# Kernel tuning notes

Hardware: AMD Instinct MI355X
Metric: run time of the kernel (lower is better)

The kernel has to match this reference:

```python
import jax, jax.numpy as jnp
import numpy as np

NUM_HEADS = 20
MAX_SEQLEN = 1500  # max per-segment length (Whisper 30s -> 1500 frames); static for jit
NEG = -1e30


def setup_inputs() -> dict:
    key = jax.random.key(0)
    ks = jax.random.split(key, 6)
    B, S, D = 4, MAX_SEQLEN, 1280
    T = B * S
    hidden_states = jax.random.normal(ks[0], (T, D), dtype=jnp.float32)
    # packed varlen layout: 4 equal-length audio segments
    cu_seqlens = (jnp.arange(B + 1, dtype=jnp.int32) * S)
    w = 0.02
    Wq = jax.random.normal(ks[1], (D, D), dtype=jnp.float32) * w
    Wk = jax.random.normal(ks[2], (D, D), dtype=jnp.float32) * w
    Wv = jax.random.normal(ks[3], (D, D), dtype=jnp.float32) * w
    Wo = jax.random.normal(ks[4], (D, D), dtype=jnp.float32) * w
    bq = jnp.zeros((D,), jnp.float32)
    bv = jnp.zeros((D,), jnp.float32)
    bo = jnp.zeros((D,), jnp.float32)
    return {"hidden_states": hidden_states, "cu_seqlens": cu_seqlens,
            "Wq": Wq, "bq": bq, "Wk": Wk, "Wv": Wv, "bv": bv, "Wo": Wo, "bo": bo}


def _varlen_attention(hidden_states, cu_seqlens, Wq, bq, Wk, Wv, bv, Wo, bo):
    T, D = hidden_states.shape
    H = NUM_HEADS
    d = D // H
    scale = d ** -0.5
    S = MAX_SEQLEN
    B = cu_seqlens.shape[0] - 1

    # projections (torch nn.Linear convention: y = x @ W.T + b; k_proj has no bias)
    q = hidden_states @ Wq.T + bq   # [T, D]
    k = hidden_states @ Wk.T        # [T, D]
    v = hidden_states @ Wv.T + bv   # [T, D]

    lens = cu_seqlens[1:] - cu_seqlens[:-1]                 # [B]
    pos = jnp.arange(S, dtype=jnp.int32)                    # [S]
    valid = pos[None, :] < lens[:, None]                    # [B, S]
    idx = cu_seqlens[:-1, None] + pos[None, :]              # [B, S]
    idx_g = jnp.where(valid, idx, 0)

    # unpack to padded [B, S, H, d]
    qb = q[idx_g].reshape(B, S, H, d)
    kb = k[idx_g].reshape(B, S, H, d)
    vb = v[idx_g].reshape(B, S, H, d)

    scores = jnp.einsum('bqhd,bkhd->bhqk', qb, kb) * scale  # [B, H, S, S]
    scores = jnp.where(valid[:, None, None, :], scores, NEG)
    attn = jax.nn.softmax(scores, axis=-1)
    out = jnp.einsum('bhqk,bkhd->bqhd', attn, vb).reshape(B, S, D)

    # repack to [T, D]; invalid slots scatter out-of-bounds and are dropped
    idx_s = jnp.where(valid, idx, T).reshape(-1)
    packed = jnp.zeros((T, D), out.dtype).at[idx_s].set(out.reshape(-1, D), mode='drop')
    return packed @ Wo.T + bo


def reference(hidden_states, cu_seqlens, Wq, bq, Wk, Wv, bv, Wo, bo):
    return _varlen_attention(hidden_states, cu_seqlens, Wq, bq, Wk, Wv, bv, Wo, bo)
```

## Files before the change

### kernel.cpp

```cpp
#include <hip/hip_runtime.h>
#include <stdint.h>
#include <math.h>

#define DMODEL 1280
#define NHEAD  20
#define DHEAD  64
#define NSEG   4
#define MAXS   1500
#define SPAD   1536
#define TPAD   (NSEG*SPAD)
#define QT256  ((MAXS + 255) / 256)
#define BM 128
#define BN 128
#define BK 32
#define QSCALE 0.18033688011112042f
#define NEGV  -1e30f

typedef float  f32x4  __attribute__((ext_vector_type(4)));
typedef __bf16 bf16x8 __attribute__((ext_vector_type(8)));

#if __has_builtin(__builtin_amdgcn_exp2f)
#define EXP2F(x) __builtin_amdgcn_exp2f(x)
#else
#define EXP2F(x) exp2f(x)
#endif

__device__ __forceinline__ ushort f2bf(float f) {
  union { float f; uint32_t u; } a; a.f = f;
  uint32_t u = a.u;
  u += 0x7FFFu + ((u >> 16) & 1u);
  return (ushort)(u >> 16);
}

__device__ __forceinline__ uint32_t pk2(float a, float b) {
  union { float f; uint32_t u; } ua, ub; ua.f = a; ub.f = b;
  uint32_t x = ua.u + 0x8000u, y = ub.u + 0x8000u;
  return (x >> 16) | (y & 0xFFFF0000u);
}

__device__ __forceinline__ void async16(const void* g, void* lds) {
  __builtin_amdgcn_global_load_lds((const __attribute__((address_space(1))) void*)g,
                                   (__attribute__((address_space(3))) void*)lds,
                                   16, 0, 0);
}

__device__ __forceinline__ int perm32(int a) {
  return ((a >> 2) & 3) * 8 + ((a >> 4) & 1) * 4 + (a & 3);
}

__global__ void __launch_bounds__(256)
cvt_all(const float* __restrict__ hs, const float* __restrict__ Wq,
        const float* __restrict__ Wk, const float* __restrict__ Wv,
        const float* __restrict__ Wo, ushort* __restrict__ dst, int nX, int DD) {
  const int i = (blockIdx.x * 256 + threadIdx.x) * 4;
  const float* src;
  if (i < nX) {
    src = hs + i;
  } else {
    int j = i - nX;
    const int z = (j >= DD) + (j >= 2 * DD) + (j >= 3 * DD);
    const float* w = (z == 0) ? Wq : (z == 1) ? Wk : (z == 2) ? Wv : Wo;
    src = w + (j - z * DD);
  }
  float4 v = *(const float4*)src;
  ushort4 o;
  o.x = f2bf(v.x); o.y = f2bf(v.y); o.z = f2bf(v.z); o.w = f2bf(v.w);
  *(ushort4*)(dst + i) = o;
}

__device__ __forceinline__ void gemm_tile_mainloop(
    const ushort* __restrict__ A, const ushort* __restrict__ W,
    int M, int m0, int n0, ushort* As, ushort* Bs, f32x4 (&acc)[4][4])
{
  const int tid  = threadIdx.x;
  const int wave = tid >> 6, lane = tid & 63;
  const int quad = lane >> 4, c16 = lane & 15;
  const int wr = (wave >> 1) * 64, wc = (wave & 1) * 64;

  const int M0 = wave * 128 + lane, M1 = M0 + 64;
  const int sr0 = M0 >> 3, pp0 = M0 & 7, p0 = pp0 ^ (sr0 & 7);
  const int sr1 = M1 >> 3, pp1 = M1 & 7, p1 = pp1 ^ (sr1 & 7);
  const int row0 = sr0 * 2 + (p0 >> 2), kc0 = (p0 & 3) << 3;
  const int row1 = sr1 * 2 + (p1 >> 2), kc1 = (p1 & 3) << 3;
  const ushort* Ap0 = A + (size_t)(m0 + row0) * DMODEL + kc0;
  const ushort* Ap1 = A + (size_t)(m0 + row1) * DMODEL + kc1;
  const ushort* Bp0 = W + (size_t)(n0 + row0) * DMODEL + kc0;
  const ushort* Bp1 = W + (size_t)(n0 + row1) * DMODEL + kc1;
  const int o0 = wave * 1024;
  const int o1 = wave * 1024 + 512;
  const int BUF = BM * BK;

  async16(Ap0, As + o0); async16(Ap1, As + o1);
  async16(Bp0, Bs + o0); async16(Bp1, Bs + o1);

  int c = 0;
  for (int k0 = 0; k0 < DMODEL; k0 += BK, c ^= 1) {
    __syncthreads();
    if (k0 + BK < DMODEL) {
      const int kn = k0 + BK;
      const int bo = (c ^ 1) * BUF;
      async16(Ap0 + kn, As + bo + o0); async16(Ap1 + kn, As + bo + o1);
      async16(Bp0 + kn, Bs + bo + o0); async16(Bp1 + kn, Bs + bo + o1);
    }
    const ushort* Ab = As + c * BUF;
    const ushort* Bb = Bs + c * BUF;
    bf16x8 a[4], b[4];
#pragma unroll
    for (int i = 0; i < 4; ++i) {
      const int row = wr + i * 16 + c16;
      const int sr = row >> 1;
      const int off = (sr << 6) + (((((row & 1) << 2) | quad) ^ (sr & 7)) << 3);
      a[i] = *(const bf16x8*)(Ab + off);
    }
#pragma unroll
    for (int j = 0; j < 4; ++j) {
      const int row = wc + j * 16 + c16;
      const int sr = row >> 1;
      const int off = (sr << 6) + (((((row & 1) << 2) | quad) ^ (sr & 7)) << 3);
      b[j] = *(const bf16x8*)(Bb + off);
    }
#pragma unroll
    for (int i = 0; i < 4; ++i)
#pragma unroll
      for (int j = 0; j < 4; ++j)
        acc[i][j] = __builtin_amdgcn_mfma_f32_16x16x32_bf16(a[i], b[j], acc[i][j], 0, 0, 0);
  }
}

__global__ void __launch_bounds__(256, 4)
gemm_qkv(const ushort* __restrict__ X, const ushort* __restrict__ W4,
         const float* __restrict__ bq, const float* __restrict__ bv,
         const int* __restrict__ cu,
         ushort* __restrict__ qb, ushort* __restrict__ kb, ushort* __restrict__ vt, int M)
{
  __shared__ ushort As[2 * BM * BK], Bs[2 * BN * BK];
  const int wg = blockIdx.x;
  if (wg >= 30) return;
  const int z = wg / 10;
  const int n0 = (wg % 10) * BN;
  const int m0 = blockIdx.y * BM;
  const ushort* W = W4 + (size_t)z * DMODEL * DMODEL;

  f32x4 acc[4][4];
  f32x4 zero = {0.f, 0.f, 0.f, 0.f};
#pragma unroll
  for (int i = 0; i < 4; ++i)
#pragma unroll
    for (int j = 0; j < 4; ++j) acc[i][j] = zero;

  gemm_tile_mainloop(X, W, M, m0, n0, As, Bs, acc);

  const int tid = threadIdx.x, wave = tid >> 6, lane = tid & 63;
  const int quad = lane >> 4, c16 = lane & 15;
  const int wr = (wave >> 1) * 64, wc = (wave & 1) * 64;

  if (z == 2) {
    const int c1 = cu[1], c2 = cu[2], c3 = cu[3];
#pragma unroll
    for (int i = 0; i < 4; ++i) {
      const int t0 = m0 + wr + i * 16 + quad * 4;
      const int s0a = (t0 >= c1) + (t0 >= c2) + (t0 >= c3);
      const int s3a = (t0 + 3 >= c1) + (t0 + 3 >= c2) + (t0 + 3 >= c3);
      const int seg0 = (s0a == 0) ? 0 : (s0a == 1) ? c1 : (s0a == 2) ? c2 : c3;
#pragma unroll
      for (int j = 0; j < 4; ++j) {
        const int cfeat = n0 + wc + j * 16 + c16;
        const float bb = bv[cfeat];
        if (t0 + 3 < M && s0a == s3a) {
          const int s = t0 - seg0;
          const size_t base = (size_t)cfeat * TPAD + (size_t)s0a * SPAD
                            + (size_t)(s & ~31) + perm32(s & 31);
          ushort4 w;
          w.x = f2bf(acc[i][j][0] + bb);
          w.y = f2bf(acc[i][j][1] + bb);
          w.z = f2bf(acc[i][j][2] + bb);
          w.w = f2bf(acc[i][j][3] + bb);
          *(ushort4*)(vt + base) = w;
        } else {
#pragma unroll
          for (int r = 0; r < 4; ++r) {
            const int t = t0 + r;
            if (t < M) {
              const int sb = (t >= c1) + (t >= c2) + (t >= c3);
              const int sg = (sb == 0) ? 0 : (sb == 1) ? c1 : (sb == 2) ? c2 : c3;
              const int s = t - sg;
              vt[(size_t)cfeat * TPAD + (size_t)sb * SPAD + (s & ~31) + perm32(s & 31)]
                  = f2bf(acc[i][j][r] + bb);
            }
          }
        }
      }
    }
  } else {
    ushort* out = (z == 0) ? qb : kb;
    const float* bias = (z == 0) ? bq : (const float*)nullptr;
    const float oscale = (z == 0) ? QSCALE : 1.0f;
#pragma unroll
    for (int i = 0; i < 4; ++i) {
      const int rbase = m0 + wr + i * 16 + quad * 4;
#pragma unroll
      for (int j = 0; j < 4; ++j) {
        const int c = n0 + wc + j * 16 + c16;
        const float bb = bias ? bias[c] : 0.f;
#pragma unroll
        for (int r = 0; r < 4; ++r) {
          const int rr = rbase + r;
          if (rr < M) out[(size_t)rr * DMODEL + c] = f2bf((acc[i][j][r] + bb) * oscale);
        }
      }
    }
  }
}

__global__ void __launch_bounds__(256, 4)
gemm_out(const ushort* __restrict__ A, const ushort* __restrict__ W,
         const float* __restrict__ bias, float* __restrict__ out, int M)
{
  __shared__ ushort As[2 * BM * BK], Bs[2 * BN * BK];
  const int wg = blockIdx.x;
  if (wg >= 10) return;
  const int n0 = wg * BN;
  const int m0 = blockIdx.y * BM;
  f32x4 acc[4][4];
  f32x4 zero = {0.f, 0.f, 0.f, 0.f};
#pragma unroll
  for (int i = 0; i < 4; ++i)
#pragma unroll
    for (int j = 0; j < 4; ++j) acc[i][j] = zero;

  gemm_tile_mainloop(A, W, M, m0, n0, As, Bs, acc);

  const int tid = threadIdx.x, wave = tid >> 6, lane = tid & 63;
  const int quad = lane >> 4, c16 = lane & 15;
  const int wr = (wave >> 1) * 64, wc = (wave & 1) * 64;
#pragma unroll
  for (int i = 0; i < 4; ++i) {
    const int rbase = m0 + wr + i * 16 + quad * 4;
#pragma unroll
    for (int j = 0; j < 4; ++j) {
      const int c = n0 + wc + j * 16 + c16;
      const float bb = bias[c];
#pragma unroll
      for (int r = 0; r < 4; ++r) {
        const int rr = rbase + r;
        if (rr < M) out[(size_t)rr * DMODEL + c] = acc[i][j][r] + bb;
      }
    }
  }
}

__global__ void __launch_bounds__(512, 4)
attn_fused(const ushort* __restrict__ qb, const ushort* __restrict__ kb,
           const ushort* __restrict__ vt, ushort* __restrict__ ob,
           const int* __restrict__ cu, int T)
{
  __shared__ ushort SB[16384];
  const int hs = blockIdx.x;
  const int b = hs / NHEAD, h = hs % NHEAD;
  const int seg0 = cu[b];
  const int len  = cu[b + 1] - seg0;
  const int q0 = blockIdx.y * 256;
  if (q0 >= len) return;
  const int tid = threadIdx.x, wave = tid >> 6, lane = tid & 63;
  const int quad = lane >> 4, c16 = lane & 15;

#pragma unroll
  for (int t = 0; t < 4; ++t) {
    const int slot = t * 512 + tid;
    const int r = slot >> 3, k2 = slot & 7;
    const int col = ((k2 ^ (r & 7)) << 3);
    async16(qb + (size_t)(seg0 + q0 + r) * DMODEL + h * DHEAD + col,
            &SB[(t * 512 + wave * 64) * 8]);
  }

  const int rK = tid >> 3, kK = tid & 7;
  const int colK = ((kK ^ (rK & 7)) << 3);
  const ushort* kp = kb + (size_t)(seg0 + rK) * DMODEL + h * DHEAD + colK;
  const ushort* vp = vt + (size_t)(h * DHEAD + rK) * TPAD + (size_t)b * SPAD + colK;
  const int ldsoff = wave * 512;

  __syncthreads();

  bf16x8 aq[2][2];
#pragma unroll
  for (int n = 0; n < 2; ++n)
#pragma unroll
    for (int ks = 0; ks < 2; ++ks) {
      const int row = wave * 32 + n * 16 + c16;
      aq[n][ks] = *(const bf16x8*)(&SB[row * 64 + (((ks * 4 + quad) ^ (c16 & 7)) << 3)]);
    }

  __syncthreads();

  async16(kp, &SB[ldsoff]); async16(vp, &SB[4096 + ldsoff]);
  kp += (size_t)64 * DMODEL; vp += 64;

  float l_i[2] = {0.f, 0.f};
  f32x4 o_acc[2][4];
  f32x4 zero = {0.f, 0.f, 0.f, 0.f};
#pragma unroll
  for (int n = 0; n < 2; ++n)
#pragma unroll
    for (int m = 0; m < 4; ++m) o_acc[n][m] = zero;

  const int niter = (len + 63) >> 6;
  for (int it = 0; it < niter; ++it) {
    __syncthreads();
    const ushort* Kt = &SB[(it & 1) * 8192];
    const ushort* Vt = Kt + 4096;

    if (it + 1 < niter) {
      ushort* Dst = &SB[((it + 1) & 1) * 8192];
      async16(kp, Dst + ldsoff); async16(vp, Dst + 4096 + ldsoff);
      kp += (size_t)64 * DMODEL; vp += 64;
    }

    f32x4 s[2][4];
    __builtin_amdgcn_s_setprio(1);
#pragma unroll
    for (int f = 0; f < 4; ++f) {
      const int row = f * 16 + c16;
      const int ch = c16 & 7;
      bf16x8 ak0 = *(const bf16x8*)(Kt + row * 64 + ((quad ^ ch) << 3));
      bf16x8 ak1 = *(const bf16x8*)(Kt + row * 64 + (((4 + quad) ^ ch) << 3));
#pragma unroll
      for (int n = 0; n < 2; ++n) {
        s[n][f] = zero;
        s[n][f] = __builtin_amdgcn_mfma_f32_16x16x32_bf16(ak0, aq[n][0], s[n][f], 0, 0, 0);
        s[n][f] = __builtin_amdgcn_mfma_f32_16x16x32_bf16(ak1, aq[n][1], s[n][f], 0, 0, 0);
      }
    }
    __builtin_amdgcn_s_setprio(0);

    const int kv0 = it * 64;
    if (kv0 + 64 > len) {
#pragma unroll
      for (int f = 0; f < 4; ++f) {
        const int kvb = kv0 + f * 16 + quad * 4;
#pragma unroll
        for (int r = 0; r < 4; ++r)
          if (kvb + r >= len) { s[0][f][r] = NEGV; s[1][f][r] = NEGV; }
      }
    }

#pragma unroll
    for (int n = 0; n < 2; ++n) {
      float rs = 0.f;
#pragma unroll
      for (int f = 0; f < 4; ++f)
#pragma unroll
        for (int r = 0; r < 4; ++r) {
          const float p = EXP2F(s[n][f][r]);
          s[n][f][r] = p;
          rs += p;
        }
      l_i[n] += rs;
    }

    bf16x8 bp[2][2];
#pragma unroll
    for (int n = 0; n < 2; ++n)
#pragma unroll
      for (int g = 0; g < 2; ++g) {
        union { uint32_t u[4]; bf16x8 v; } cv;
        cv.u[0] = pk2(s[n][2 * g][0], s[n][2 * g][1]);
        cv.u[1] = pk2(s[n][2 * g][2], s[n][2 * g][3]);
        cv.u[2] = pk2(s[n][2 * g + 1][0], s[n][2 * g + 1][1]);
        cv.u[3] = pk2(s[n][2 * g + 1][2], s[n][2 * g + 1][3]);
        bp[n][g] = cv.v;
      }

    __builtin_amdgcn_s_setprio(1);
#pragma unroll
    for (int m = 0; m < 4; ++m) {
      const int row = m * 16 + c16;
      const int ch = c16 & 7;
      bf16x8 av0 = *(const bf16x8*)(Vt + row * 64 + ((quad ^ ch) << 3));
      bf16x8 av1 = *(const bf16x8*)(Vt + row * 64 + (((4 + quad) ^ ch) << 3));
#pragma unroll
      for (int n = 0; n < 2; ++n) {
        o_acc[n][m] = __builtin_amdgcn_mfma_f32_16x16x32_bf16(av0, bp[n][0], o_acc[n][m], 0, 0, 0);
        o_acc[n][m] = __builtin_amdgcn_mfma_f32_16x16x32_bf16(av1, bp[n][1], o_acc[n][m], 0, 0, 0);
      }
    }
    __builtin_amdgcn_s_setprio(0);
  }

#pragma unroll
  for (int n = 0; n < 2; ++n) {
    float l = l_i[n];
    l += __shfl_xor(l, 16);
    l += __shfl_xor(l, 32);
    const int q = q0 + wave * 32 + n * 16 + c16;
    if (q < len) {
      const float inv = 1.0f / l;
      const size_t base = (size_t)(seg0 + q) * DMODEL + h * DHEAD;
#pragma unroll
      for (int m = 0; m < 4; ++m) {
        ushort4 pk;
        pk.x = f2bf(o_acc[n][m][0] * inv);
        pk.y = f2bf(o_acc[n][m][1] * inv);
        pk.z = f2bf(o_acc[n][m][2] * inv);
        pk.w = f2bf(o_acc[n][m][3] * inv);
        *(ushort4*)(ob + base + m * 16 + quad * 4) = pk;
      }
    }
  }
}

extern "C" void kernel_launch(void* const* d_in, const int* in_sizes, int n_in,
                              void* d_out, int out_size, void* d_ws, size_t ws_size,
                              hipStream_t stream)
{
  (void)n_in; (void)out_size; (void)ws_size;
  const float* hs = (const float*)d_in[0];
  const int*   cu = (const int*)d_in[1];
  const float* Wq = (const float*)d_in[2];
  const float* bq = (const float*)d_in[3];
  const float* Wk = (const float*)d_in[4];
  const float* Wv = (const float*)d_in[5];
  const float* bv = (const float*)d_in[6];
  const float* Wo = (const float*)d_in[7];
  const float* bo = (const float*)d_in[8];
  float* out = (float*)d_out;
  const int T  = in_sizes[0] / DMODEL;
  const int DD = DMODEL * DMODEL;
  const int nX = T * DMODEL;

  ushort* ws  = (ushort*)d_ws;
  ushort* X   = ws;
  ushort* W4  = X + (size_t)nX;
  ushort* qb  = W4 + 4 * (size_t)DD;
  ushort* kb  = qb + (size_t)T * DMODEL;
  ushort* vt  = kb + (size_t)T * DMODEL;
  ushort* ob  = X;

  const int ncvt = nX + 4 * DD;
  cvt_all<<<(ncvt / 4 + 255) / 256, 256, 0, stream>>>(hs, Wq, Wk, Wv, Wo, ws, nX, DD);

  gemm_qkv<<<dim3(32, (T + BM - 1) / BM), 256, 0, stream>>>(
      X, W4, bq, bv, cu, qb, kb, vt, T);

  attn_fused<<<dim3(NSEG * NHEAD, QT256), 512, 0, stream>>>(qb, kb, vt, ob, cu, T);

  gemm_out<<<dim3(16, (T + BM - 1) / BM), 256, 0, stream>>>(
      ob, W4 + 3 * (size_t)DD, bo, out, T);
}
```

Before: 303.3 us.

## Rewrite QKV GEMM with 256x256 tiles, 512 threads, XCD-aware block mapping

Replaces the 128x128 QKV projection GEMM with a 256x256 tile, BK=64 kernel using 8 waves, direct global-to-LDS async loads with an XOR swizzle, and an explicit double-buffered pipeline. A 1D grid of 360 blocks is remapped so that consecutive tiles land on the same XCD, which should improve L2 reuse. The larger tiles raise arithmetic intensity and cut redundant loads of A and B. In exchange, register and LDS use per block go up, occupancy drops, and M=6000 is padded up to 24 tiles of 256 rows, so the last tile reads out-of-range rows.

After: 315.8 us. 1.04x slower.

```diff
diff --git a/kernel.cpp b/kernel.cpp
--- a/kernel.cpp
+++ b/kernel.cpp
@@ -13,6 +13,10 @@
 #define BM 128
 #define BN 128
 #define BK 32
+#define BM2 256
+#define BN2 256
+#define BKQ 64
+#define NT2 (DMODEL / BKQ)
 #define QSCALE 0.18033688011112042f
 #define NEGV  -1e30f
 
@@ -47,6 +51,16 @@
 __device__ __forceinline__ int perm32(int a) {
   return ((a >> 2) & 3) * 8 + ((a >> 4) & 1) * 4 + (a & 3);
 }
+
+__device__ __forceinline__ int xcd_chunk(int d, int nwg) {
+  const int q = nwg >> 3, r = nwg & 7;
+  const int x = d & 7, pos = d >> 3;
+  return (x < r ? x * (q + 1) : r * (q + 1) + (x - r) * q) + pos;
+}
+
+#define GBAR()  do { asm volatile("" ::: "memory"); __builtin_amdgcn_s_barrier(); \
+                     asm volatile("" ::: "memory"); } while (0)
+#define WAITV(n) asm volatile("s_waitcnt vmcnt(" #n ")" ::: "memory")
 
 __global__ void __launch_bounds__(256)
 cvt_all(const float* __restrict__ hs, const float* __restrict__ Wq,
@@ -127,37 +141,107 @@
   }
 }
 
-__global__ void __launch_bounds__(256, 4)
+__global__ void __launch_bounds__(512, 2)
 gemm_qkv(const ushort* __restrict__ X, const ushort* __restrict__ W4,
          const float* __restrict__ bq, const float* __restrict__ bv,
          const int* __restrict__ cu,
          ushort* __restrict__ qb, ushort* __restrict__ kb, ushort* __restrict__ vt, int M)
 {
-  __shared__ ushort As[2 * BM * BK], Bs[2 * BN * BK];
-  const int wg = blockIdx.x;
-  if (wg >= 30) return;
-  const int z = wg / 10;
-  const int n0 = (wg % 10) * BN;
-  const int m0 = blockIdx.y * BM;
+  __shared__ __align__(16) ushort As[2 * 16384];
+  __shared__ __align__(16) ushort Bs[2 * 16384];
+  const int lid = xcd_chunk(blockIdx.x, 360);
+  const int zn = lid / 24, mt = lid - zn * 24;
+  const int z = zn / 5, nn = zn - z * 5;
+  const int n0 = nn * BN2, m0 = mt * BM2;
   const ushort* W = W4 + (size_t)z * DMODEL * DMODEL;
-
-  f32x4 acc[4][4];
-  f32x4 zero = {0.f, 0.f, 0.f, 0.f};
-#pragma unroll
-  for (int i = 0; i < 4; ++i)
-#pragma unroll
-    for (int j = 0; j < 4; ++j) acc[i][j] = zero;
-
-  gemm_tile_mainloop(X, W, M, m0, n0, As, Bs, acc);
 
   const int tid = threadIdx.x, wave = tid >> 6, lane = tid & 63;
   const int quad = lane >> 4, c16 = lane & 15;
-  const int wr = (wave >> 1) * 64, wc = (wave & 1) * 64;
+  const int wr = (wave >> 2) * 128, wc = (wave & 3) * 64;
+
+  const ushort* ApS0; const ushort* ApS1; const ushort* ApS2; const ushort* ApS3;
+  const ushort* BpS0; const ushort* BpS1; const ushort* BpS2; const ushort* BpS3;
+  int ldsS0, ldsS1, ldsS2, ldsS3;
+#define SDECODE(q, Ap, Bp, Ld) do { \
+    const int s = (q) * 512 + wave * 64 + lane; \
+    const int r = s >> 3, p = s & 7; \
+    const int gc = (p ^ (r & 7)) << 3; \
+    Ap = X + (size_t)(m0 + r) * DMODEL + gc; \
+    Bp = W + (size_t)(n0 + r) * DMODEL + gc; \
+    Ld = ((q) * 512 + wave * 64) * 8; \
+  } while (0)
+  SDECODE(0, ApS0, BpS0, ldsS0);
+  SDECODE(1, ApS1, BpS1, ldsS1);
+  SDECODE(2, ApS2, BpS2, ldsS2);
+  SDECODE(3, ApS3, BpS3, ldsS3);
+#undef SDECODE
+
+#define STAGE(b, kk) do { \
+    ushort* Ad = As + (b) * 16384; ushort* Bd = Bs + (b) * 16384; \
+    async16(ApS0 + (kk), Ad + ldsS0); async16(BpS0 + (kk), Bd + ldsS0); \
+    async16(ApS1 + (kk), Ad + ldsS1); async16(BpS1 + (kk), Bd + ldsS1); \
+    async16(ApS2 + (kk), Ad + ldsS2); async16(BpS2 + (kk), Bd + ldsS2); \
+    async16(ApS3 + (kk), Ad + ldsS3); async16(BpS3 + (kk), Bd + ldsS3); \
+  } while (0)
+
+  f32x4 acc[8][4];
+  f32x4 zero = {0.f, 0.f, 0.f, 0.f};
+#pragma unroll
+  for (int i = 0; i < 8; ++i)
+#pragma unroll
+    for (int j = 0; j < 4; ++j) acc[i][j] = zero;
+
+#define COMPUTE(b) do { \
+    const ushort* Ab = As + (b) * 16384; \
+    const ushort* Bb = Bs + (b) * 16384; \
+    _Pragma("unroll") \
+    for (int ks = 0; ks < 2; ++ks) { \
+      bf16x8 a[8], bb[4]; \
+      _Pragma("unroll") \
+      for (int i = 0; i < 8; ++i) { \
+        const int row = wr + i * 16 + c16; \
+        a[i] = *(const bf16x8*)(Ab + row * 64 + ((((ks << 2) | quad) ^ (row & 7)) << 3)); \
+      } \
+      _Pragma("unroll") \
+      for (int j = 0; j < 4; ++j) { \
+        const int row = wc + j * 16 + c16; \
+        bb[j] = *(const bf16x8*)(Bb + row * 64 + ((((ks << 2) | quad) ^ (row & 7)) << 3)); \
+      } \
+      _Pragma("unroll") \
+      for (int i = 0; i < 8; ++i) \
+        _Pragma("unroll") \
+        for (int j = 0; j < 4; ++j) \
+          acc[i][j] = __builtin_amdgcn_mfma_f32_16x16x32_bf16(a[i], bb[j], acc[i][j], 0, 0, 0); \
+    } \
+  } while (0)
+
+  STAGE(0, 0);
+  STAGE(1, BKQ);
+  WAITV(8);
+  GBAR();
+
+#pragma unroll 1
+  for (int t = 0; t < NT2; t += 2) {
+    COMPUTE(0);
+    GBAR();
+    if (t + 2 < NT2) { STAGE(0, (t + 2) * BKQ); WAITV(8); }
+    else             { WAITV(0); }
+    GBAR();
+    COMPUTE(1);
+    if (t + 2 < NT2) {
+      GBAR();
+      if (t + 3 < NT2) { STAGE(1, (t + 3) * BKQ); WAITV(8); }
+      else             { WAITV(0); }
+      GBAR();
+    }
+  }
+#undef COMPUTE
+#undef STAGE
 
   if (z == 2) {
     const int c1 = cu[1], c2 = cu[2], c3 = cu[3];
 #pragma unroll
-    for (int i = 0; i < 4; ++i) {
+    for (int i = 0; i < 8; ++i) {
       const int t0 = m0 + wr + i * 16 + quad * 4;
       const int s0a = (t0 >= c1) + (t0 >= c2) + (t0 >= c3);
       const int s3a = (t0 + 3 >= c1) + (t0 + 3 >= c2) + (t0 + 3 >= c3);
@@ -196,7 +280,7 @@
     const float* bias = (z == 0) ? bq : (const float*)nullptr;
     const float oscale = (z == 0) ? QSCALE : 1.0f;
 #pragma unroll
-    for (int i = 0; i < 4; ++i) {
+    for (int i = 0; i < 8; ++i) {
       const int rbase = m0 + wr + i * 16 + quad * 4;
 #pragma unroll
       for (int j = 0; j < 4; ++j) {
@@ -438,8 +522,7 @@
   const int ncvt = nX + 4 * DD;
   cvt_all<<<(ncvt / 4 + 255) / 256, 256, 0, stream>>>(hs, Wq, Wk, Wv, Wo, ws, nX, DD);
 
-  gemm_qkv<<<dim3(32, (T + BM - 1) / BM), 256, 0, stream>>>(
-      X, W4, bq, bv, cu, qb, kb, vt, T);
+  gemm_qkv<<<360, 512, 0, stream>>>(X, W4, bq, bv, cu, qb, kb, vt, T);
 
   attn_fused<<<dim3(NSEG * NHEAD, QT256), 512, 0, stream>>>(qb, kb, vt, ob, cu, T);
 
```
